# Kernel tuning notes

Hardware: AMD Instinct MI355X
Metric: run time of the kernel (lower is better)

The kernel has to match this reference:

```python
import jax, jax.numpy as jnp
import numpy as np

B, T, F, H, E, CTX = 64, 400, 80, 256, 256, 20


def setup_inputs() -> dict:
    ks = iter(jax.random.split(jax.random.key(0), 40))

    def p(shape):
        return jax.random.normal(next(ks), shape, jnp.float32) * 0.1

    inp = {"x": p((B, T, F))}
    inp["emb_W"], inp["emb_b"] = p((E, F)), p((E,))
    for name, din, dh in [("e1", F, H), ("e2", H, H), ("e3", H, H),
                          ("d1", 2 * E, H), ("d2", H, H), ("d3", H, F)]:
        inp[name + "_Wih"] = p((4 * dh, din))
        inp[name + "_Whh"] = p((4 * dh, dh))
        inp[name + "_b"] = p((4 * dh,))  # fused b_ih + b_hh
    inp["key_W"], inp["key_b"] = p((E, H)), p((E,))
    inp["val_W"], inp["val_b"] = p((E, H)), p((E,))
    inp["epoch"] = 5  # unused when isTrain=False (no teacher forcing)
    return inp


def _lstm(xin, hc, Wih, Whh, b):
    h, c = hc
    g = xin @ Wih.T + h @ Whh.T + b
    i, f, gg, o = jnp.split(g, 4, axis=-1)  # torch gate order i,f,g,o
    c = jax.nn.sigmoid(f) * c + jax.nn.sigmoid(i) * jnp.tanh(gg)
    h = jax.nn.sigmoid(o) * jnp.tanh(c)
    return (h, c)


def _forward(x, emb_W, emb_b, e1_Wih, e1_Whh, e1_b, e2_Wih, e2_Whh, e2_b,
             e3_Wih, e3_Whh, e3_b, d1_Wih, d1_Whh, d1_b, d2_Wih, d2_Whh, d2_b,
             d3_Wih, d3_Whh, d3_b, key_W, key_b, val_W, val_b):
    Bb = x.shape[0]
    z = lambda d: (jnp.zeros((Bb, d), x.dtype), jnp.zeros((Bb, d), x.dtype))

    def encoder(enc, xin):
        e1, e2, e3 = enc
        e1 = _lstm(xin, e1, e1_Wih, e1_Whh, e1_b)
        e2 = _lstm(e1[0], e2, e2_Wih, e2_Whh, e2_b)
        e3 = _lstm(e2[0], e3, e3_Wih, e3_Whh, e3_b)
        k = e3[0] @ key_W.T + key_b
        v = e3[0] @ val_W.T + val_b
        return (e1, e2, e3), k, v

    def decoder(dec, emb, ctx):
        d1, d2, d3 = dec
        din = jnp.concatenate([emb, ctx], axis=-1)  # [B, 2E]
        d1 = _lstm(din, d1, d1_Wih, d1_Whh, d1_b)
        d2 = _lstm(d1[0], d2, d2_Wih, d2_Whh, d2_b)
        d3 = _lstm(d2[0], d3, d3_Wih, d3_Whh, d3_b)
        return (d1, d2, d3)

    # phase 1: encoder warmup over steps 0..CTX-1
    def p1(enc, xt):
        enc, k, v = encoder(enc, xt)
        return enc, (k, v)

    enc, (ks_, vs_) = jax.lax.scan(p1, (z(H), z(H), z(H)),
                                   jnp.swapaxes(x[:, :CTX], 0, 1))
    kbuf = jnp.swapaxes(ks_, 0, 1)  # [B, CTX, E]: keys for steps 0..CTX-1
    vbuf = jnp.swapaxes(vs_, 0, 1)

    # step i == CTX: first decoder step; context = current value (values[-1])
    enc, k20, v20 = encoder(enc, x[:, CTX])
    kbuf = jnp.concatenate([kbuf[:, 1:], k20[:, None]], axis=1)
    vbuf = jnp.concatenate([vbuf[:, 1:], v20[:, None]], axis=1)
    emb = x[:, CTX - 1] @ emb_W.T + emb_b
    dec = decoder((z(H), z(H), z(F)), emb, v20)
    out20 = dec[2][0]  # [B, F]

    def p2(carry, _):
        enc, dec, kbuf, vbuf, last = carry
        enc, k, v = encoder(enc, last)           # encoder_input = prev decoder out
        emb = last @ emb_W.T + emb_b             # embedding of prev decoder out
        q = dec[1][0]                            # decoder2 hidden from prev step
        attn = jax.nn.softmax(jnp.einsum('bke,be->bk', kbuf, q), axis=-1)
        ctx = jnp.einsum('bk,bke->be', attn, vbuf)
        dec = decoder(dec, emb, ctx)
        kbuf = jnp.concatenate([kbuf[:, 1:], k[:, None]], axis=1)
        vbuf = jnp.concatenate([vbuf[:, 1:], v[:, None]], axis=1)
        out = dec[2][0]
        return (enc, dec, kbuf, vbuf, out), out

    _, outs = jax.lax.scan(p2, (enc, dec, kbuf, vbuf, out20), None,
                           length=T - CTX - 1)
    # [B, T-CTX, F] = [B, 380, 80]
    return jnp.concatenate([out20[:, None], jnp.swapaxes(outs, 0, 1)], axis=1)


def reference(x, emb_W, emb_b, e1_Wih, e1_Whh, e1_b, e2_Wih, e2_Whh, e2_b,
              e3_Wih, e3_Whh, e3_b, d1_Wih, d1_Whh, d1_b, d2_Wih, d2_Whh, d2_b,
              d3_Wih, d3_Whh, d3_b, key_W, key_b, val_W, val_b, epoch):
    return _forward(x, emb_W, emb_b, e1_Wih, e1_Whh, e1_b, e2_Wih, e2_Whh, e2_b,
                    e3_Wih, e3_Whh, e3_b, d1_Wih, d1_Whh, d1_b, d2_Wih, d2_Whh,
                    d2_b, d3_Wih, d3_Whh, d3_b, key_W, key_b, val_W, val_b)
```

## Files before the change

### kernel.cpp

```cpp
#include <hip/hip_runtime.h>

typedef short bf16x8 __attribute__((ext_vector_type(8)));
typedef float f32x4 __attribute__((ext_vector_type(4)));

#define DEV static __device__ __forceinline__
#define SCOPE_AGENT __HIP_MEMORY_SCOPE_AGENT

DEV unsigned short f2bf(float f) {
  unsigned u = __float_as_uint(f);
  unsigned r = u + 0x7fffu + ((u >> 16) & 1u);
  return (unsigned short)(r >> 16);
}
DEV float bf2f(unsigned short h) { return __uint_as_float(((unsigned)h) << 16); }
DEV void f2hilo(float f, unsigned short& hi, unsigned short& lo) {
  hi = f2bf(f);
  lo = f2bf(f - bf2f(hi));
}
DEV float sigm(float x) { return 1.f / (1.f + __expf(-x)); }
DEV float tanh_(float x) {
  x = fminf(15.f, fmaxf(-15.f, x));
  float e = __expf(2.f * x);
  return (e - 1.f) / (e + 1.f);
}

DEV void st_sc_u16(unsigned short* p, unsigned short v) {
  __hip_atomic_store(p, v, __ATOMIC_RELAXED, SCOPE_AGENT);
}
DEV void st_sc_f32(float* p, float v) {
  __hip_atomic_store(p, v, __ATOMIC_RELAXED, SCOPE_AGENT);
}
DEV void st_sc_u64(unsigned long long* p, unsigned long long v) {
  __hip_atomic_store(p, v, __ATOMIC_RELAXED, SCOPE_AGENT);
}
DEV unsigned long long ld_sc_u64(const unsigned long long* p) {
  return __hip_atomic_load((unsigned long long*)p, __ATOMIC_RELAXED, SCOPE_AGENT);
}
DEV unsigned ld_sc_u32(const unsigned* p) {
  return __hip_atomic_load((unsigned*)p, __ATOMIC_RELAXED, SCOPE_AGENT);
}
DEV void vm_drain() { asm volatile("s_waitcnt vmcnt(0)" ::: "memory"); }

constexpr size_t WE1 = 1024 * 352, WE2 = 1024 * 512, WE3 = 1024 * 512,
                 WD1 = 1024 * 768, WD2 = 1024 * 512, WD3 = 320 * 352,
                 WKEY = 256 * 256, WVAL = 256 * 256, WEMB = 256 * 96;
constexpr size_t E1HI = 0, E1LO = E1HI + WE1, E2HI = E1LO + WE1, E2LO = E2HI + WE2,
                 E3HI = E2LO + WE2, E3LO = E3HI + WE3, D1HI = E3LO + WE3, D1LO = D1HI + WD1,
                 D2HI = D1LO + WD1, D2LO = D2HI + WD2, D3HI = D2LO + WD2, D3LO = D3HI + WD3,
                 KHI = D3LO + WD3, KLO = KHI + WKEY, VHI = KLO + WKEY, VLO = VHI + WVAL,
                 EMHI = VLO + WVAL, EMLO = EMHI + WEMB, WTOT = EMLO + WEMB;

constexpr size_t XPAD_ELEMS = (size_t)400 * 64 * 96;
constexpr size_t XPAD_HI_B = WTOT * 2;
constexpr size_t XPAD_LO_B = XPAD_HI_B + XPAD_ELEMS * 2;
constexpr size_t STATE_B = XPAD_LO_B + XPAD_ELEMS * 2;

constexpr size_t H256_SZB = (size_t)2 * 2 * 64 * 256 * 2;
constexpr size_t HE1 = 0, HE2 = H256_SZB, HE3 = 2 * H256_SZB, HD1 = 3 * H256_SZB,
                 HD2 = 4 * H256_SZB;
constexpr size_t HLAST = 5 * H256_SZB;
constexpr size_t HLAST_SZB = (size_t)2 * 2 * 64 * 96 * 2;
constexpr size_t BARO = HLAST + HLAST_SZB;
constexpr size_t STATE_BYTES = BARO + 9 * 400 * 4 + 64;

constexpr size_t RINGK_B = STATE_B + STATE_BYTES;
constexpr size_t RING_SZ = (size_t)22 * 64 * 256 * 4;
constexpr size_t RINGV_B = RINGK_B + RING_SZ;
constexpr size_t CTXH_B = RINGV_B + RING_SZ;
constexpr size_t CTXL_B = CTXH_B + (size_t)64 * 256 * 2;
constexpr size_t D1BP_B = CTXL_B + (size_t)64 * 256 * 2;
constexpr size_t WS_NEED = D1BP_B + 4096;

#define LE1 0
#define LE2 1
#define LE3 2
#define LKV 3
#define LAT 5
#define LD1 6
#define LD2 7
#define LD3 8

constexpr int NWG = 67;
constexpr int WGS = 256;

__global__ void prep_w(const float* __restrict__ wih, int din, const float* __restrict__ whh,
                       int dh, int rows, int dinp, int kp, unsigned short* __restrict__ whi,
                       unsigned short* __restrict__ wlo) {
  size_t idx = (size_t)blockIdx.x * 256 + threadIdx.x;
  size_t tot = (size_t)rows * kp;
  if (idx >= tot) return;
  int j = (int)(idx / kp), k = (int)(idx % kp);
  float v = 0.f;
  if (k < dinp) {
    if (k < din) v = wih[(size_t)j * din + k];
  } else {
    int k2 = k - dinp;
    if (k2 < dh) v = whh[(size_t)j * dh + k2];
  }
  unsigned short hi, lo;
  f2hilo(v, hi, lo);
  whi[idx] = hi;
  wlo[idx] = lo;
}

__global__ void prep_d1_w(const float* __restrict__ wih, const float* __restrict__ whh,
                          const float* __restrict__ embW, unsigned short* __restrict__ whi,
                          unsigned short* __restrict__ wlo) {
  size_t idx = (size_t)blockIdx.x * 256 + threadIdx.x;
  constexpr size_t tot = (size_t)1024 * 608;
  if (idx >= tot) return;
  int j = (int)(idx / 608), f = (int)(idx % 608);
  float v = 0.f;
  if (f < 96) {
    if (f < 80) {
      const float* wr = wih + (size_t)j * 512;
#pragma unroll 4
      for (int m = 0; m < 256; m++) v += wr[m] * embW[(size_t)m * 80 + f];
    }
  } else if (f < 352) {
    v = wih[(size_t)j * 512 + 256 + (f - 96)];
  } else {
    v = whh[(size_t)j * 256 + (f - 352)];
  }
  unsigned short hi, lo;
  f2hilo(v, hi, lo);
  whi[idx] = hi;
  wlo[idx] = lo;
}

__global__ void prep_d1_bias(const float* __restrict__ wih, const float* __restrict__ embb,
                             const float* __restrict__ d1b, float* __restrict__ out) {
  int j = blockIdx.x * 256 + threadIdx.x;
  if (j >= 1024) return;
  float v = d1b[j];
  const float* wr = wih + (size_t)j * 512;
#pragma unroll 4
  for (int m = 0; m < 256; m++) v += wr[m] * embb[m];
  out[j] = v;
}

__global__ void prep_x(const float* __restrict__ x, unsigned short* __restrict__ xh,
                       unsigned short* __restrict__ xl) {
  size_t idx = (size_t)blockIdx.x * 256 + threadIdx.x;
  if (idx >= XPAD_ELEMS) return;
  int t = (int)(idx / 6144), rbf = (int)(idx % 6144), b = rbf / 96, f = rbf % 96;
  float v = (f < 80) ? x[(size_t)b * 32000 + (size_t)t * 80 + f] : 0.f;
  unsigned short hi, lo;
  f2hilo(v, hi, lo);
  xh[idx] = hi;
  xl[idx] = lo;
}


template <int COLS, int STRIDE>
DEV void copy_hl(unsigned short* lds, const unsigned short* hi, const unsigned short* lo,
                 int tid) {
  constexpr int CU64 = COLS / 4;
  constexpr int PER = 64 * CU64;
  constexpr int TOT = PER * 2;
  constexpr int loOff = 64 * STRIDE;
  for (int base = 0; base < TOT; base += WGS * 16) {
    unsigned long long v[16];
    int dst[16];
#pragma unroll
    for (int u = 0; u < 16; u++) {
      int i = base + u * WGS + tid;
      dst[u] = -1;
      if (i < TOT) {
        int pl = (i >= PER) ? 1 : 0;
        int j = pl ? (i - PER) : i;
        int row = j / CU64, cc = j - row * CU64;
        const unsigned long long* s = (const unsigned long long*)(pl ? lo : hi);
        v[u] = ld_sc_u64(s + j);
        dst[u] = (pl ? loOff : 0) + row * STRIDE + ((cc * 4) ^ ((row & 7) << 3));
      }
    }
#pragma unroll
    for (int u = 0; u < 16; u++)
      if (dst[u] >= 0) *(unsigned long long*)(lds + dst[u]) = v[u];
  }
}

DEV void mfma3(f32x4& acc, bf16x8 ah, bf16x8 al, bf16x8 bh, bf16x8 bl) {
  acc = __builtin_amdgcn_mfma_f32_16x16x32_bf16(ah, bh, acc, 0, 0, 0);
  acc = __builtin_amdgcn_mfma_f32_16x16x32_bf16(al, bh, acc, 0, 0, 0);
  acc = __builtin_amdgcn_mfma_f32_16x16x32_bf16(ah, bl, acc, 0, 0, 0);
}

DEV void zacc44(f32x4 (&a)[4][4]) {
#pragma unroll
  for (int g = 0; g < 4; g++)
#pragma unroll
    for (int m = 0; m < 4; m++) a[g][m] = f32x4{0.f, 0.f, 0.f, 0.f};
}

template <int STRIDE>
DEV void mfma_range(const unsigned short* lds, int lane, int ut, int H,
                    const unsigned short* __restrict__ Whi,
                    const unsigned short* __restrict__ Wlo, int Kp, int kwOff, int kbLo,
                    int kbHi, f32x4 (&acc)[4][4]) {
  const int col = lane & 15, kg = lane >> 4;
  constexpr int loOff = 64 * STRIDE;
  for (int kb = kbLo; kb < kbHi; kb++) {
    const int ka = kb * 32 + kg * 8;
    bf16x8 ah[4], al[4];
#pragma unroll
    for (int m = 0; m < 4; m++) {
      int row = m * 16 + col;
      int off = row * STRIDE + (ka ^ ((row & 7) << 3));
      ah[m] = *(const bf16x8*)(lds + off);
      al[m] = *(const bf16x8*)(lds + loOff + off);
    }
#pragma unroll
    for (int g = 0; g < 4; g++) {
      size_t wr = (size_t)(g * H + ut * 16 + col) * Kp + kwOff + ka;
      bf16x8 bh = *(const bf16x8*)(Whi + wr);
      bf16x8 bl = *(const bf16x8*)(Wlo + wr);
#pragma unroll
      for (int m = 0; m < 4; m++) mfma3(acc[g][m], ah[m], al[m], bh, bl);
    }
  }
}

template <int COLS, int STRIDE>
DEV void chunk_pass(unsigned short* lds, const unsigned short* hi, const unsigned short* lo,
                    int tid, int lane, int ut, int utActive, int H,
                    const unsigned short* __restrict__ Whi,
                    const unsigned short* __restrict__ Wlo, int Kp, int kwOff, int half,
                    f32x4 (&acc)[4][4]) {
  __syncthreads();
  copy_hl<COLS, STRIDE>(lds, hi, lo, tid);
  __syncthreads();
  constexpr int NKB = COLS / 32;
  const int lo_kb = half ? (NKB + 1) / 2 : 0;
  const int hi_kb = half ? NKB : (NKB + 1) / 2;
  if (utActive) mfma_range<STRIDE>(lds, lane, ut, H, Whi, Wlo, Kp, kwOff, lo_kb, hi_kb, acc);
}

DEV void reduce_pair(unsigned short* lds, int lane, int pair, int half, f32x4 (&acc)[4][4]) {
  float* red = (float*)lds;
  const int base = (pair * 64 + lane) * 68;
  __syncthreads();
  if (half) {
#pragma unroll
    for (int g = 0; g < 4; g++)
#pragma unroll
      for (int m = 0; m < 4; m++)
#pragma unroll
        for (int r = 0; r < 4; r++) red[base + (g * 4 + m) * 4 + r] = acc[g][m][r];
  }
  __syncthreads();
  if (!half) {
#pragma unroll
    for (int g = 0; g < 4; g++)
#pragma unroll
      for (int m = 0; m < 4; m++)
#pragma unroll
        for (int r = 0; r < 4; r++) acc[g][m][r] += red[base + (g * 4 + m) * 4 + r];
  }
}

DEV void cell_update(int lane, int ut, int H, int Hpad, const float* __restrict__ bias,
                     f32x4 (&acc)[4][4], float (&c)[4][4], unsigned short* hwhi,
                     unsigned short* hwlo, float* outp) {
  const int col = lane & 15, kg = lane >> 4;
  const int u = ut * 16 + col;
  const float bi = bias[u], bff = bias[H + u], bg = bias[2 * H + u], bo = bias[3 * H + u];
#pragma unroll
  for (int m = 0; m < 4; m++)
#pragma unroll
    for (int r = 0; r < 4; r++) {
      int b = m * 16 + kg * 4 + r;
      float gi = acc[0][m][r] + bi, gf = acc[1][m][r] + bff;
      float gg = acc[2][m][r] + bg, go = acc[3][m][r] + bo;
      float cn = sigm(gf) * c[m][r] + sigm(gi) * tanh_(gg);
      float hh = sigm(go) * tanh_(cn);
      c[m][r] = cn;
      unsigned short hi, lo;
      f2hilo(hh, hi, lo);
      st_sc_u16(hwhi + b * Hpad + u, hi);
      st_sc_u16(hwlo + b * Hpad + u, lo);
      if (outp) outp[(size_t)b * 30400 + u] = hh;
    }
}

template <int K, int STRIDE>
DEV void mfma_lin(const unsigned short* lds, int lane, int jt,
                  const unsigned short* __restrict__ Whi,
                  const unsigned short* __restrict__ Wlo, int Kp, f32x4 (&acc)[4]) {
  const int col = lane & 15, kg = lane >> 4;
  constexpr int loOff = 64 * STRIDE;
#pragma unroll
  for (int kb = 0; kb < K; kb += 32) {
    const int ka = kb + kg * 8;
    size_t wr = (size_t)(jt * 16 + col) * Kp + ka;
    bf16x8 bh = *(const bf16x8*)(Whi + wr);
    bf16x8 bl = *(const bf16x8*)(Wlo + wr);
#pragma unroll
    for (int m = 0; m < 4; m++) {
      int row = m * 16 + col;
      int off = row * STRIDE + (ka ^ ((row & 7) << 3));
      bf16x8 ah = *(const bf16x8*)(lds + off);
      bf16x8 al = *(const bf16x8*)(lds + loOff + off);
      mfma3(acc[m], ah, al, bh, bl);
    }
  }
}

DEV void spin3(const unsigned* p0, unsigned t0, const unsigned* p1, unsigned t1,
               const unsigned* p2, unsigned t2) {
  for (;;) {
    unsigned a = p0 ? ld_sc_u32(p0) : 0xFFFFFFFFu;
    unsigned b = p1 ? ld_sc_u32(p1) : 0xFFFFFFFFu;
    unsigned c = p2 ? ld_sc_u32(p2) : 0xFFFFFFFFu;
    if (a >= t0 && b >= t1 && c >= t2) return;
    __builtin_amdgcn_s_sleep(1);
  }
}

__global__ void __launch_bounds__(WGS, 1)
seq_main(const float* e1b, const float* e2b, const float* e3b, const float* d2b,
         const float* d3b, const float* keyb, const float* valb, float* dout,
         unsigned char* ws) {
  __shared__ unsigned short lds_s[32768];
  unsigned short* lds = lds_s;

  const int wg = blockIdx.x, tid = threadIdx.x;
  const int wv = tid >> 6, lane = tid & 63;
  const int pair = wv >> 1, half = wv & 1;

  unsigned short* W = (unsigned short*)ws;
  const unsigned short* xh = (const unsigned short*)(ws + XPAD_HI_B);
  const unsigned short* xl = (const unsigned short*)(ws + XPAD_LO_B);
  unsigned char* st = ws + STATE_B;
  float* ringk = (float*)(ws + RINGK_B);
  float* ringv = (float*)(ws + RINGV_B);
  unsigned short* ctxh = (unsigned short*)(ws + CTXH_B);
  unsigned short* ctxl = (unsigned short*)(ws + CTXL_B);
  const float* d1bp = (const float*)(ws + D1BP_B);
  unsigned* C = (unsigned*)(st + BARO);
  auto CNT = [&](int l, int tt) { return C + l * 400 + tt; };

  auto hb = [&](size_t off, int par, int hl, int Hpad) {
    return (unsigned short*)(st + off) + (size_t)(par * 2 + hl) * 64 * Hpad;
  };
  auto bump = [&](int l, int tt) {
    if (tid == 0) __hip_atomic_fetch_add(CNT(l, tt), 1u, __ATOMIC_RELAXED, SCOPE_AGENT);
  };

  if (wg < 8) {
    const int ut = wg * 2 + pair;
    float c[4][4] = {{0.f}};
    for (int t = 0; t < 400; ++t) {
      const int p = t & 1, q = p ^ 1;
      f32x4 acc[4][4];
      zacc44(acc);
      if (tid == 0 && t >= 1) spin3(CNT(LE1, t - 1), 8, nullptr, 0, nullptr, 0);
      chunk_pass<256, 256>(lds, hb(HE1, q, 0, 256), hb(HE1, q, 1, 256), tid, lane, ut, 1, 256,
                           W + E1HI, W + E1LO, 352, 96, half, acc);
      if (tid == 0)
        spin3(t >= 21 ? CNT(LD3, t - 1) : nullptr, 3, t >= 2 ? CNT(LE2, t - 2) : nullptr, 8,
              nullptr, 0);
      if (t <= 20)
        chunk_pass<96, 128>(lds, xh + (size_t)t * 6144, xl + (size_t)t * 6144, tid, lane, ut, 1,
                            256, W + E1HI, W + E1LO, 352, 0, half, acc);
      else
        chunk_pass<96, 128>(lds, hb(HLAST, q, 0, 96), hb(HLAST, q, 1, 96), tid, lane, ut, 1,
                            256, W + E1HI, W + E1LO, 352, 0, half, acc);
      reduce_pair(lds, lane, pair, half, acc);
      if (!half)
        cell_update(lane, ut, 256, 256, e1b, acc, c, hb(HE1, p, 0, 256), hb(HE1, p, 1, 256),
                    nullptr);
      vm_drain();
      __syncthreads();
      bump(LE1, t);
    }
  } else if (wg < 16) {
    const int ut = (wg - 8) * 2 + pair;
    float c[4][4] = {{0.f}};
    for (int t = 0; t < 400; ++t) {
      const int p = t & 1, q = p ^ 1;
      f32x4 acc[4][4];
      zacc44(acc);
      if (tid == 0 && t >= 1) spin3(CNT(LE2, t - 1), 8, nullptr, 0, nullptr, 0);
      chunk_pass<256, 256>(lds, hb(HE2, q, 0, 256), hb(HE2, q, 1, 256), tid, lane, ut, 1, 256,
                           W + E2HI, W + E2LO, 512, 256, half, acc);
      if (tid == 0)
        spin3(CNT(LE1, t), 8, t >= 2 ? CNT(LE3, t - 2) : nullptr, 8, nullptr, 0);
      chunk_pass<256, 256>(lds, hb(HE1, p, 0, 256), hb(HE1, p, 1, 256), tid, lane, ut, 1, 256,
                           W + E2HI, W + E2LO, 512, 0, half, acc);
      reduce_pair(lds, lane, pair, half, acc);
      if (!half)
        cell_update(lane, ut, 256, 256, e2b, acc, c, hb(HE2, p, 0, 256), hb(HE2, p, 1, 256),
                    nullptr);
      vm_drain();
      __syncthreads();
      bump(LE2, t);
    }
  } else if (wg < 24) {
    const int ut = (wg - 16) * 2 + pair;
    float c[4][4] = {{0.f}};
    for (int t = 0; t < 400; ++t) {
      const int p = t & 1, q = p ^ 1;
      f32x4 acc[4][4];
      zacc44(acc);
      if (tid == 0 && t >= 1) spin3(CNT(LE3, t - 1), 8, nullptr, 0, nullptr, 0);
      chunk_pass<256, 256>(lds, hb(HE3, q, 0, 256), hb(HE3, q, 1, 256), tid, lane, ut, 1, 256,
                           W + E3HI, W + E3LO, 512, 256, half, acc);
      if (tid == 0)
        spin3(CNT(LE2, t), 8, t >= 2 ? CNT(LKV, t - 2) : nullptr, 8, nullptr, 0);
      chunk_pass<256, 256>(lds, hb(HE2, p, 0, 256), hb(HE2, p, 1, 256), tid, lane, ut, 1, 256,
                           W + E3HI, W + E3LO, 512, 0, half, acc);
      reduce_pair(lds, lane, pair, half, acc);
      if (!half)
        cell_update(lane, ut, 256, 256, e3b, acc, c, hb(HE3, p, 0, 256), hb(HE3, p, 1, 256),
                    nullptr);
      vm_drain();
      __syncthreads();
      bump(LE3, t);
    }
  } else if (wg < 32) {
    const bool isKey = wg < 28;
    const unsigned short* Whi = W + (isKey ? KHI : VHI);
    const unsigned short* Wlo = W + (isKey ? KLO : VLO);
    const float* bias = isKey ? keyb : valb;
    float* ring = isKey ? ringk : ringv;
    const int jt = (wg - (isKey ? 24 : 28)) * 4 + wv;
    const int col = lane & 15, kg = lane >> 4;
    for (int t = 0; t < 400; ++t) {
      const int p = t & 1;
      const int slot = t % 22;
      if (tid == 0)
        spin3(CNT(LE3, t), 8, t >= 22 ? CNT(LAT, t - 2) : nullptr, 16, nullptr, 0);
      __syncthreads();
      copy_hl<256, 256>(lds, hb(HE3, p, 0, 256), hb(HE3, p, 1, 256), tid);
      __syncthreads();
      float* outp = ring + (size_t)slot * 64 * 256;
      f32x4 acc[4];
#pragma unroll
      for (int m = 0; m < 4; m++) acc[m] = f32x4{0.f, 0.f, 0.f, 0.f};
      mfma_lin<256, 256>(lds, lane, jt, Whi, Wlo, 256, acc);
      int j = jt * 16 + col;
      float bj = bias[j];
#pragma unroll
      for (int m = 0; m < 4; m++)
#pragma unroll
        for (int r = 0; r < 4; r++) {
          int b = m * 16 + kg * 4 + r;
          st_sc_f32(outp + (size_t)b * 256 + j, acc[m][r] + bj);
        }
      vm_drain();
      __syncthreads();
      bump(LKV, t);
    }
  } else if (wg < 48) {
    const int b = (wg - 32) * 4 + wv;
    for (int t = 20; t < 400; ++t) {
      const int q = (t & 1) ^ 1;
      if (t == 20) {
        if (tid == 0) spin3(CNT(LKV, 20), 8, nullptr, 0, nullptr, 0);
        __syncthreads();
        const unsigned long long* vp =
            (const unsigned long long*)(ringv + ((size_t)20 * 64 + b) * 256 + lane * 4);
        unsigned long long v0 = ld_sc_u64(vp), v1 = ld_sc_u64(vp + 1);
        float f[4] = {__uint_as_float((unsigned)v0), __uint_as_float((unsigned)(v0 >> 32)),
                      __uint_as_float((unsigned)v1), __uint_as_float((unsigned)(v1 >> 32))};
        unsigned short hi[4], lo[4];
#pragma unroll
        for (int j = 0; j < 4; j++) f2hilo(f[j], hi[j], lo[j]);
        unsigned long long ph = (unsigned long long)hi[0] | ((unsigned long long)hi[1] << 16) |
                                ((unsigned long long)hi[2] << 32) |
                                ((unsigned long long)hi[3] << 48);
        unsigned long long pl = (unsigned long long)lo[0] | ((unsigned long long)lo[1] << 16) |
                                ((unsigned long long)lo[2] << 32) |
                                ((unsigned long long)lo[3] << 48);
        st_sc_u64((unsigned long long*)(ctxh + b * 256 + lane * 4), ph);
        st_sc_u64((unsigned long long*)(ctxl + b * 256 + lane * 4), pl);
      } else {
        if (tid == 0)
          spin3(CNT(LKV, t - 1), 8, CNT(LD2, t - 1), 8, CNT(LD1, t - 1), 8);
        __syncthreads();
        const unsigned short* qh = hb(HD2, q, 0, 256);
        const unsigned short* ql = hb(HD2, q, 1, 256);
        unsigned long long hq = ld_sc_u64((const unsigned long long*)(qh + b * 256 + lane * 4));
        unsigned long long lq = ld_sc_u64((const unsigned long long*)(ql + b * 256 + lane * 4));
        float qv[4];
#pragma unroll
        for (int j = 0; j < 4; j++)
          qv[j] = bf2f((unsigned short)(hq >> (16 * j))) + bf2f((unsigned short)(lq >> (16 * j)));
        float s[20];
#pragma unroll
        for (int i = 0; i < 20; i++) {
          int slot = (t - 20 + i) % 22;
          const unsigned long long* kp =
              (const unsigned long long*)(ringk + ((size_t)slot * 64 + b) * 256 + lane * 4);
          unsigned long long k0 = ld_sc_u64(kp), k1 = ld_sc_u64(kp + 1);
          s[i] = __uint_as_float((unsigned)k0) * qv[0] +
                 __uint_as_float((unsigned)(k0 >> 32)) * qv[1] +
                 __uint_as_float((unsigned)k1) * qv[2] +
                 __uint_as_float((unsigned)(k1 >> 32)) * qv[3];
        }
#pragma unroll
        for (int off = 32; off >= 1; off >>= 1)
#pragma unroll
          for (int i = 0; i < 20; i++) s[i] += __shfl_xor(s[i], off, 64);
        float mx = s[0];
#pragma unroll
        for (int i = 1; i < 20; i++) mx = fmaxf(mx, s[i]);
        float den = 0.f;
#pragma unroll
        for (int i = 0; i < 20; i++) {
          s[i] = __expf(s[i] - mx);
          den += s[i];
        }
        float inv = 1.f / den;
        float a0 = 0.f, a1 = 0.f, a2 = 0.f, a3 = 0.f;
#pragma unroll
        for (int i = 0; i < 20; i++) {
          int slot = (t - 20 + i) % 22;
          const unsigned long long* vp =
              (const unsigned long long*)(ringv + ((size_t)slot * 64 + b) * 256 + lane * 4);
          unsigned long long v0 = ld_sc_u64(vp), v1 = ld_sc_u64(vp + 1);
          a0 += s[i] * __uint_as_float((unsigned)v0);
          a1 += s[i] * __uint_as_float((unsigned)(v0 >> 32));
          a2 += s[i] * __uint_as_float((unsigned)v1);
          a3 += s[i] * __uint_as_float((unsigned)(v1 >> 32));
        }
        float f[4] = {a0 * inv, a1 * inv, a2 * inv, a3 * inv};
        unsigned short hi[4], lo[4];
#pragma unroll
        for (int j = 0; j < 4; j++) f2hilo(f[j], hi[j], lo[j]);
        unsigned long long ph = (unsigned long long)hi[0] | ((unsigned long long)hi[1] << 16) |
                                ((unsigned long long)hi[2] << 32) |
                                ((unsigned long long)hi[3] << 48);
        unsigned long long pl = (unsigned long long)lo[0] | ((unsigned long long)lo[1] << 16) |
                                ((unsigned long long)lo[2] << 32) |
                                ((unsigned long long)lo[3] << 48);
        st_sc_u64((unsigned long long*)(ctxh + b * 256 + lane * 4), ph);
        st_sc_u64((unsigned long long*)(ctxl + b * 256 + lane * 4), pl);
      }
      vm_drain();
      __syncthreads();
      bump(LAT, t);
    }
  } else if (wg < 56) {
    const int ut = (wg - 48) * 2 + pair;
    float c[4][4] = {{0.f}};
    for (int t = 20; t < 400; ++t) {
      const int p = t & 1, q = p ^ 1;
      f32x4 acc[4][4];
      zacc44(acc);
      if (tid == 0 && t >= 21) spin3(CNT(LD1, t - 1), 8, nullptr, 0, nullptr, 0);
      chunk_pass<256, 256>(lds, hb(HD1, q, 0, 256), hb(HD1, q, 1, 256), tid, lane, ut, 1, 256,
                           W + D1HI, W + D1LO, 608, 352, half, acc);
      if (tid == 0 && t >= 21) spin3(CNT(LD3, t - 1), 3, nullptr, 0, nullptr, 0);
      if (t == 20)
        chunk_pass<96, 128>(lds, xh + (size_t)19 * 6144, xl + (size_t)19 * 6144, tid, lane, ut,
                            1, 256, W + D1HI, W + D1LO, 608, 0, half, acc);
      else
        chunk_pass<96, 128>(lds, hb(HLAST, q, 0, 96), hb(HLAST, q, 1, 96), tid, lane, ut, 1,
                            256, W + D1HI, W + D1LO, 608, 0, half, acc);
      if (tid == 0) spin3(CNT(LAT, t), 16, nullptr, 0, nullptr, 0);
      chunk_pass<256, 256>(lds, ctxh, ctxl, tid, lane, ut, 1, 256, W + D1HI, W + D1LO, 608, 96,
                           half, acc);
      reduce_pair(lds, lane, pair, half, acc);
      if (!half)
        cell_update(lane, ut, 256, 256, d1bp, acc, c, hb(HD1, p, 0, 256), hb(HD1, p, 1, 256),
                    nullptr);
      vm_drain();
      __syncthreads();
      bump(LD1, t);
    }
  } else if (wg < 64) {
    const int ut = (wg - 56) * 2 + pair;
    float c[4][4] = {{0.f}};
    for (int t = 20; t < 400; ++t) {
      const int p = t & 1, q = p ^ 1;
      f32x4 acc[4][4];
      zacc44(acc);
      if (tid == 0 && t >= 21) spin3(CNT(LD2, t - 1), 8, nullptr, 0, nullptr, 0);
      chunk_pass<256, 256>(lds, hb(HD2, q, 0, 256), hb(HD2, q, 1, 256), tid, lane, ut, 1, 256,
                           W + D2HI, W + D2LO, 512, 256, half, acc);
      if (tid == 0) spin3(CNT(LD1, t), 8, nullptr, 0, nullptr, 0);
      chunk_pass<256, 256>(lds, hb(HD1, p, 0, 256), hb(HD1, p, 1, 256), tid, lane, ut, 1, 256,
                           W + D2HI, W + D2LO, 512, 0, half, acc);
      reduce_pair(lds, lane, pair, half, acc);
      if (!half)
        cell_update(lane, ut, 256, 256, d2b, acc, c, hb(HD2, p, 0, 256), hb(HD2, p, 1, 256),
                    nullptr);
      vm_drain();
      __syncthreads();
      bump(LD2, t);
    }
  } else {
    const int ut = (wg - 64) * 2 + pair;
    const int utActive = (ut < 5) ? 1 : 0;
    float c[4][4] = {{0.f}};
    for (int t = 20; t < 400; ++t) {
      const int p = t & 1, q = p ^ 1;
      f32x4 acc[4][4];
      zacc44(acc);
      if (tid == 0 && t >= 21) spin3(CNT(LD3, t - 1), 3, nullptr, 0, nullptr, 0);
      chunk_pass<96, 128>(lds, hb(HLAST, q, 0, 96), hb(HLAST, q, 1, 96), tid, lane, ut, utActive,
                          80, W + D3HI, W + D3LO, 352, 256, half, acc);
      if (tid == 0) spin3(CNT(LD2, t), 8, nullptr, 0, nullptr, 0);
      chunk_pass<256, 256>(lds, hb(HD2, p, 0, 256), hb(HD2, p, 1, 256), tid, lane, ut, utActive,
                           80, W + D3HI, W + D3LO, 352, 0, half, acc);
      reduce_pair(lds, lane, pair, half, acc);
      if (!half && utActive)
        cell_update(lane, ut, 80, 96, d3b, acc, c, hb(HLAST, p, 0, 96), hb(HLAST, p, 1, 96),
                    dout + (size_t)(t - 20) * 80);
      vm_drain();
      __syncthreads();
      bump(LD3, t);
    }
  }
}

extern "C" void kernel_launch(void* const* d_in, const int* in_sizes, int n_in, void* d_out,
                              int out_size, void* d_ws, size_t ws_size, hipStream_t stream) {
  if (ws_size < WS_NEED) return;

  const float* x = (const float*)d_in[0];
  const float* embW = (const float*)d_in[1];
  const float* embB = (const float*)d_in[2];
  const float* e1Wih = (const float*)d_in[3];
  const float* e1Whh = (const float*)d_in[4];
  const float* e1B = (const float*)d_in[5];
  const float* e2Wih = (const float*)d_in[6];
  const float* e2Whh = (const float*)d_in[7];
  const float* e2B = (const float*)d_in[8];
  const float* e3Wih = (const float*)d_in[9];
  const float* e3Whh = (const float*)d_in[10];
  const float* e3B = (const float*)d_in[11];
  const float* d1Wih = (const float*)d_in[12];
  const float* d1Whh = (const float*)d_in[13];
  const float* d1B = (const float*)d_in[14];
  const float* d2Wih = (const float*)d_in[15];
  const float* d2Whh = (const float*)d_in[16];
  const float* d2B = (const float*)d_in[17];
  const float* d3Wih = (const float*)d_in[18];
  const float* d3Whh = (const float*)d_in[19];
  const float* d3B = (const float*)d_in[20];
  const float* keyW = (const float*)d_in[21];
  const float* keyB = (const float*)d_in[22];
  const float* valW = (const float*)d_in[23];
  const float* valB = (const float*)d_in[24];

  unsigned char* ws = (unsigned char*)d_ws;
  unsigned short* W = (unsigned short*)ws;
  float* doutf = (float*)d_out;

  auto launch_w = [&](const float* wih, int din, const float* whh, int dh, int rows, int dinp,
                      int kp, size_t offhi, size_t offlo) {
    size_t tot = (size_t)rows * kp;
    int blocks = (int)((tot + 255) / 256);
    prep_w<<<blocks, 256, 0, stream>>>(wih, din, whh, dh, rows, dinp, kp, W + offhi, W + offlo);
  };
  launch_w(e1Wih, 80, e1Whh, 256, 1024, 96, 352, E1HI, E1LO);
  launch_w(e2Wih, 256, e2Whh, 256, 1024, 256, 512, E2HI, E2LO);
  launch_w(e3Wih, 256, e3Whh, 256, 1024, 256, 512, E3HI, E3LO);
  launch_w(d2Wih, 256, d2Whh, 256, 1024, 256, 512, D2HI, D2LO);
  launch_w(d3Wih, 256, d3Whh, 80, 320, 256, 352, D3HI, D3LO);
  launch_w(keyW, 256, nullptr, 0, 256, 256, 256, KHI, KLO);
// ... 14 lines not shown
```

Before: 14.99 ms.

## Fuse key/value projection into attention workgroups, partitioned by batch

Replaces the separate key/value projection stage (8 workgroups) with projection work done inside the 16 attention workgroups, each handling 4 batch rows. Each attention workgroup computes K/V for its own batch rows, keeps the newest step's K/V in LDS, and uses that LDS copy for the latest attention slot. This removes a cross-workgroup barrier hop and ring round-trip on the critical path. The trade-off is that the projection now runs serially inside the attention step, and encoder3 gains a wait on attention progress. The copy_hl unroll is also doubled.

```diff
diff --git a/kernel.cpp b/kernel.cpp
--- a/kernel.cpp
+++ b/kernel.cpp
@@ -73,13 +73,12 @@
 #define LE1 0
 #define LE2 1
 #define LE3 2
-#define LKV 3
 #define LAT 5
 #define LD1 6
 #define LD2 7
 #define LD3 8
 
-constexpr int NWG = 67;
+constexpr int NWG = 59;
 constexpr int WGS = 256;
 
 __global__ void prep_w(const float* __restrict__ wih, int din, const float* __restrict__ whh,
@@ -158,11 +157,11 @@
   constexpr int PER = 64 * CU64;
   constexpr int TOT = PER * 2;
   constexpr int loOff = 64 * STRIDE;
-  for (int base = 0; base < TOT; base += WGS * 16) {
-    unsigned long long v[16];
-    int dst[16];
-#pragma unroll
-    for (int u = 0; u < 16; u++) {
+  for (int base = 0; base < TOT; base += WGS * 32) {
+    unsigned long long v[32];
+    int dst[32];
+#pragma unroll
+    for (int u = 0; u < 32; u++) {
       int i = base + u * WGS + tid;
       dst[u] = -1;
       if (i < TOT) {
@@ -175,7 +174,7 @@
       }
     }
 #pragma unroll
-    for (int u = 0; u < 16; u++)
+    for (int u = 0; u < 32; u++)
       if (dst[u] >= 0) *(unsigned long long*)(lds + dst[u]) = v[u];
   }
 }
@@ -281,29 +280,6 @@
       st_sc_u16(hwlo + b * Hpad + u, lo);
       if (outp) outp[(size_t)b * 30400 + u] = hh;
     }
-}
-
-template <int K, int STRIDE>
-DEV void mfma_lin(const unsigned short* lds, int lane, int jt,
-                  const unsigned short* __restrict__ Whi,
-                  const unsigned short* __restrict__ Wlo, int Kp, f32x4 (&acc)[4]) {
-  const int col = lane & 15, kg = lane >> 4;
-  constexpr int loOff = 64 * STRIDE;
-#pragma unroll
-  for (int kb = 0; kb < K; kb += 32) {
-    const int ka = kb + kg * 8;
-    size_t wr = (size_t)(jt * 16 + col) * Kp + ka;
-    bf16x8 bh = *(const bf16x8*)(Whi + wr);
-    bf16x8 bl = *(const bf16x8*)(Wlo + wr);
-#pragma unroll
-    for (int m = 0; m < 4; m++) {
-      int row = m * 16 + col;
-      int off = row * STRIDE + (ka ^ ((row & 7) << 3));
-      bf16x8 ah = *(const bf16x8*)(lds + off);
-      bf16x8 al = *(const bf16x8*)(lds + loOff + off);
-      mfma3(acc[m], ah, al, bh, bl);
-    }
-  }
 }
 
 DEV void spin3(const unsigned* p0, unsigned t0, const unsigned* p1, unsigned t1,
@@ -406,11 +382,12 @@
       if (tid == 0 && t >= 1) spin3(CNT(LE3, t - 1), 8, nullptr, 0, nullptr, 0);
       chunk_pass<256, 256>(lds, hb(HE3, q, 0, 256), hb(HE3, q, 1, 256), tid, lane, ut, 1, 256,
                            W + E3HI, W + E3LO, 512, 256, half, acc);
-      if (tid == 0)
-        spin3(CNT(LE2, t), 8, t >= 2 ? CNT(LKV, t - 2) : nullptr, 8, nullptr, 0);
+      if (tid == 0) spin3(CNT(LE2, t), 8, nullptr, 0, nullptr, 0);
       chunk_pass<256, 256>(lds, hb(HE2, p, 0, 256), hb(HE2, p, 1, 256), tid, lane, ut, 1, 256,
                            W + E3HI, W + E3LO, 512, 0, half, acc);
       reduce_pair(lds, lane, pair, half, acc);
+      if (tid == 0 && t >= 1) spin3(CNT(LAT, t - 1), 16, nullptr, 0, nullptr, 0);
+      __syncthreads();
       if (!half)
         cell_update(lane, ut, 256, 256, e3b, acc, c, hb(HE3, p, 0, 256), hb(HE3, p, 1, 256),
                     nullptr);
@@ -418,52 +395,66 @@
       __syncthreads();
       bump(LE3, t);
     }
-  } else if (wg < 32) {
-    const bool isKey = wg < 28;
-    const unsigned short* Whi = W + (isKey ? KHI : VHI);
-    const unsigned short* Wlo = W + (isKey ? KLO : VLO);
-    const float* bias = isKey ? keyb : valb;
-    float* ring = isKey ? ringk : ringv;
-    const int jt = (wg - (isKey ? 24 : 28)) * 4 + wv;
-    const int col = lane & 15, kg = lane >> 4;
+  } else if (wg < 40) {
+    const int b0 = (wg - 24) * 4;
+    float* kvx = (float*)(lds + 8192);
     for (int t = 0; t < 400; ++t) {
-      const int p = t & 1;
-      const int slot = t % 22;
-      if (tid == 0)
-        spin3(CNT(LE3, t), 8, t >= 22 ? CNT(LAT, t - 2) : nullptr, 16, nullptr, 0);
-      __syncthreads();
-      copy_hl<256, 256>(lds, hb(HE3, p, 0, 256), hb(HE3, p, 1, 256), tid);
-      __syncthreads();
-      float* outp = ring + (size_t)slot * 64 * 256;
-      f32x4 acc[4];
-#pragma unroll
-      for (int m = 0; m < 4; m++) acc[m] = f32x4{0.f, 0.f, 0.f, 0.f};
-      mfma_lin<256, 256>(lds, lane, jt, Whi, Wlo, 256, acc);
-      int j = jt * 16 + col;
-      float bj = bias[j];
-#pragma unroll
-      for (int m = 0; m < 4; m++)
-#pragma unroll
-        for (int r = 0; r < 4; r++) {
-          int b = m * 16 + kg * 4 + r;
-          st_sc_f32(outp + (size_t)b * 256 + j, acc[m][r] + bj);
+      const int s = (t <= 20) ? t : t - 1;
+      const int ps = s & 1;
+      const bool doKV = (t != 21);
+      if (tid == 0) {
+        if (t <= 20)
+          spin3(CNT(LE3, t), 8, nullptr, 0, nullptr, 0);
+        else
+          spin3(CNT(LE3, t - 1), 8, CNT(LD2, t - 1), 8, CNT(LD1, t - 1), 8);
+      }
+      __syncthreads();
+      if (doKV) {
+        for (int i = tid; i < 512; i += WGS) {
+          int pl = i >> 8, j = i & 255, row = j >> 6, cc = j & 63;
+          const unsigned long long* srcp =
+              (const unsigned long long*)hb(HE3, ps, pl, 256) + (size_t)(b0 + row) * 64 + cc;
+          unsigned long long v = ld_sc_u64(srcp);
+          *(unsigned long long*)(lds + pl * 4096 + row * 256 +
+                                 ((cc * 4) ^ ((row & 7) << 3))) = v;
         }
-      vm_drain();
-      __syncthreads();
-      bump(LKV, t);
-    }
-  } else if (wg < 48) {
-    const int b = (wg - 32) * 4 + wv;
-    for (int t = 20; t < 400; ++t) {
-      const int q = (t & 1) ^ 1;
+        __syncthreads();
+        const int slot = s % 22;
+        const int col = lane & 15, kg = lane >> 4;
+        for (int jj = 0; jj < 8; ++jj) {
+          int jt = wv * 8 + jj;
+          bool isK = jt < 16;
+          int j = (isK ? jt : jt - 16) * 16 + col;
+          const unsigned short* Whi = W + (isK ? KHI : VHI);
+          const unsigned short* Wlo = W + (isK ? KLO : VLO);
+          f32x4 acc = f32x4{0.f, 0.f, 0.f, 0.f};
+          for (int kb = 0; kb < 8; kb++) {
+            int ka = kb * 32 + kg * 8;
+            int offA = col * 256 + (ka ^ ((col & 7) << 3));
+            bf16x8 ah = *(const bf16x8*)(lds + offA);
+            bf16x8 al = *(const bf16x8*)(lds + 4096 + offA);
+            size_t wr = (size_t)j * 256 + ka;
+            bf16x8 bh = *(const bf16x8*)(Whi + wr);
+            bf16x8 bl = *(const bf16x8*)(Wlo + wr);
+            mfma3(acc, ah, al, bh, bl);
+          }
+          if (kg == 0) {
+            float bj = (isK ? keyb : valb)[j];
+            float* ringp = (isK ? ringk : ringv) + (size_t)slot * 64 * 256;
+#pragma unroll
+            for (int r = 0; r < 4; r++) {
+              float v = acc[r] + bj;
+              st_sc_f32(ringp + (size_t)(b0 + r) * 256 + j, v);
+              kvx[r * 512 + (isK ? j : 256 + j)] = v;
+            }
+          }
+        }
+        __syncthreads();
+      }
       if (t == 20) {
-        if (tid == 0) spin3(CNT(LKV, 20), 8, nullptr, 0, nullptr, 0);
-        __syncthreads();
-        const unsigned long long* vp =
-            (const unsigned long long*)(ringv + ((size_t)20 * 64 + b) * 256 + lane * 4);
-        unsigned long long v0 = ld_sc_u64(vp), v1 = ld_sc_u64(vp + 1);
-        float f[4] = {__uint_as_float((unsigned)v0), __uint_as_float((unsigned)(v0 >> 32)),
-                      __uint_as_float((unsigned)v1), __uint_as_float((unsigned)(v1 >> 32))};
+        float f[4];
+#pragma unroll
+        for (int j = 0; j < 4; j++) f[j] = kvx[wv * 512 + 256 + lane * 4 + j];
         unsigned short hi[4], lo[4];
 #pragma unroll
         for (int j = 0; j < 4; j++) f2hilo(f[j], hi[j], lo[j]);
@@ -473,58 +464,67 @@
         unsigned long long pl = (unsigned long long)lo[0] | ((unsigned long long)lo[1] << 16) |
                                 ((unsigned long long)lo[2] << 32) |
                                 ((unsigned long long)lo[3] << 48);
-        st_sc_u64((unsigned long long*)(ctxh + b * 256 + lane * 4), ph);
-        st_sc_u64((unsigned long long*)(ctxl + b * 256 + lane * 4), pl);
-      } else {
-        if (tid == 0)
-          spin3(CNT(LKV, t - 1), 8, CNT(LD2, t - 1), 8, CNT(LD1, t - 1), 8);
-        __syncthreads();
-        const unsigned short* qh = hb(HD2, q, 0, 256);
-        const unsigned short* ql = hb(HD2, q, 1, 256);
+        st_sc_u64((unsigned long long*)(ctxh + (b0 + wv) * 256 + lane * 4), ph);
+        st_sc_u64((unsigned long long*)(ctxl + (b0 + wv) * 256 + lane * 4), pl);
+      } else if (t >= 21) {
+        const int b = b0 + wv;
+        const int qp = (t & 1) ^ 1;
+        const unsigned short* qh = hb(HD2, qp, 0, 256);
+        const unsigned short* ql = hb(HD2, qp, 1, 256);
         unsigned long long hq = ld_sc_u64((const unsigned long long*)(qh + b * 256 + lane * 4));
         unsigned long long lq = ld_sc_u64((const unsigned long long*)(ql + b * 256 + lane * 4));
         float qv[4];
 #pragma unroll
         for (int j = 0; j < 4; j++)
           qv[j] = bf2f((unsigned short)(hq >> (16 * j))) + bf2f((unsigned short)(lq >> (16 * j)));
-        float s[20];
-#pragma unroll
-        for (int i = 0; i < 20; i++) {
+        float sArr[20];
+#pragma unroll
+        for (int i = 0; i < 19; i++) {
           int slot = (t - 20 + i) % 22;
           const unsigned long long* kp =
               (const unsigned long long*)(ringk + ((size_t)slot * 64 + b) * 256 + lane * 4);
           unsigned long long k0 = ld_sc_u64(kp), k1 = ld_sc_u64(kp + 1);
-          s[i] = __uint_as_float((unsigned)k0) * qv[0] +
-                 __uint_as_float((unsigned)(k0 >> 32)) * qv[1] +
-                 __uint_as_float((unsigned)k1) * qv[2] +
-                 __uint_as_float((unsigned)(k1 >> 32)) * qv[3];
+          sArr[i] = __uint_as_float((unsigned)k0) * qv[0] +
+                    __uint_as_float((unsigned)(k0 >> 32)) * qv[1] +
+                    __uint_as_float((unsigned)k1) * qv[2] +
+                    __uint_as_float((unsigned)(k1 >> 32)) * qv[3];
         }
+        {
+          float acc19 = 0.f;
+#pragma unroll
+          for (int j = 0; j < 4; j++) acc19 += kvx[wv * 512 + lane * 4 + j] * qv[j];
+          sArr[19] = acc19;
+        }
 #pragma unroll
         for (int off = 32; off >= 1; off >>= 1)
 #pragma unroll
-          for (int i = 0; i < 20; i++) s[i] += __shfl_xor(s[i], off, 64);
-        float mx = s[0];
-#pragma unroll
-        for (int i = 1; i < 20; i++) mx = fmaxf(mx, s[i]);
+          for (int i = 0; i < 20; i++) sArr[i] += __shfl_xor(sArr[i], off, 64);
+        float mx = sArr[0];
+#pragma unroll
+        for (int i = 1; i < 20; i++) mx = fmaxf(mx, sArr[i]);
         float den = 0.f;
 #pragma unroll
         for (int i = 0; i < 20; i++) {
-          s[i] = __expf(s[i] - mx);
-          den += s[i];
+          sArr[i] = __expf(sArr[i] - mx);
+          den += sArr[i];
         }
         float inv = 1.f / den;
         float a0 = 0.f, a1 = 0.f, a2 = 0.f, a3 = 0.f;
 #pragma unroll
-        for (int i = 0; i < 20; i++) {
+        for (int i = 0; i < 19; i++) {
           int slot = (t - 20 + i) % 22;
           const unsigned long long* vp =
               (const unsigned long long*)(ringv + ((size_t)slot * 64 + b) * 256 + lane * 4);
           unsigned long long v0 = ld_sc_u64(vp), v1 = ld_sc_u64(vp + 1);
-          a0 += s[i] * __uint_as_float((unsigned)v0);
-          a1 += s[i] * __uint_as_float((unsigned)(v0 >> 32));
-          a2 += s[i] * __uint_as_float((unsigned)v1);
-          a3 += s[i] * __uint_as_float((unsigned)(v1 >> 32));
+          a0 += sArr[i] * __uint_as_float((unsigned)v0);
+          a1 += sArr[i] * __uint_as_float((unsigned)(v0 >> 32));
+          a2 += sArr[i] * __uint_as_float((unsigned)v1);
+          a3 += sArr[i] * __uint_as_float((unsigned)(v1 >> 32));
         }
+        a0 += sArr[19] * kvx[wv * 512 + 256 + lane * 4 + 0];
+        a1 += sArr[19] * kvx[wv * 512 + 256 + lane * 4 + 1];
+        a2 += sArr[19] * kvx[wv * 512 + 256 + lane * 4 + 2];
+        a3 += sArr[19] * kvx[wv * 512 + 256 + lane * 4 + 3];
         float f[4] = {a0 * inv, a1 * inv, a2 * inv, a3 * inv};
         unsigned short hi[4], lo[4];
 #pragma unroll
@@ -542,8 +542,8 @@
       __syncthreads();
       bump(LAT, t);
     }
-  } else if (wg < 56) {
-    const int ut = (wg - 48) * 2 + pair;
+  } else if (wg < 48) {
+    const int ut = (wg - 40) * 2 + pair;
     float c[4][4] = {{0.f}};
     for (int t = 20; t < 400; ++t) {
       const int p = t & 1, q = p ^ 1;
@@ -570,8 +570,8 @@
       __syncthreads();
       bump(LD1, t);
     }
-  } else if (wg < 64) {
-    const int ut = (wg - 56) * 2 + pair;
+  } else if (wg < 56) {
+    const int ut = (wg - 48) * 2 + pair;
     float c[4][4] = {{0.f}};
     for (int t = 20; t < 400; ++t) {
       const int p = t & 1, q = p ^ 1;
@@ -592,7 +592,7 @@
       bump(LD2, t);
     }
   } else {
-    const int ut = (wg - 64) * 2 + pair;
+    const int ut = (wg - 56) * 2 + pair;
     const int utActive = (ut < 5) ? 1 : 0;
     float c[4][4] = {{0.f}};
     for (int t = 20; t < 400; ++t) {
```

New measurement: 18.30 ms. +22.1%, slower.

## Stage LSTM hidden outputs in LDS, double-buffer context, and relax attention dependency

Applied to the files above, without the earlier changes.

Hidden-state outputs from the LSTM cell update are first written to an LDS staging area and then stored to global memory as coalesced 64-bit writes, replacing scattered 16-bit stores. The attention context buffer is double-buffered by timestep parity, so the attention workgroups no longer wait for decoder layer 1 of the previous step before overwriting the context. The LDS copy loop is also unrolled to 32 loads per pass. These changes target global store efficiency and the serial dependency chain on the recurrent critical path, at the cost of an extra barrier per step and more registers in the copy loop.

```diff
diff --git a/kernel.cpp b/kernel.cpp
--- a/kernel.cpp
+++ b/kernel.cpp
@@ -66,8 +66,8 @@
 constexpr size_t RING_SZ = (size_t)22 * 64 * 256 * 4;
 constexpr size_t RINGV_B = RINGK_B + RING_SZ;
 constexpr size_t CTXH_B = RINGV_B + RING_SZ;
-constexpr size_t CTXL_B = CTXH_B + (size_t)64 * 256 * 2;
-constexpr size_t D1BP_B = CTXL_B + (size_t)64 * 256 * 2;
+constexpr size_t CTXL_B = CTXH_B + (size_t)2 * 64 * 256 * 2;
+constexpr size_t D1BP_B = CTXL_B + (size_t)2 * 64 * 256 * 2;
 constexpr size_t WS_NEED = D1BP_B + 4096;
 
 #define LE1 0
@@ -81,6 +81,7 @@
 
 constexpr int NWG = 67;
 constexpr int WGS = 256;
+constexpr int HSTG = 20480;
 
 __global__ void prep_w(const float* __restrict__ wih, int din, const float* __restrict__ whh,
                        int dh, int rows, int dinp, int kp, unsigned short* __restrict__ whi,
@@ -158,11 +159,11 @@
   constexpr int PER = 64 * CU64;
   constexpr int TOT = PER * 2;
   constexpr int loOff = 64 * STRIDE;
-  for (int base = 0; base < TOT; base += WGS * 16) {
-    unsigned long long v[16];
-    int dst[16];
-#pragma unroll
-    for (int u = 0; u < 16; u++) {
+  for (int base = 0; base < TOT; base += WGS * 32) {
+    unsigned long long v[32];
+    int dst[32];
+#pragma unroll
+    for (int u = 0; u < 32; u++) {
       int i = base + u * WGS + tid;
       dst[u] = -1;
       if (i < TOT) {
@@ -175,7 +176,7 @@
       }
     }
 #pragma unroll
-    for (int u = 0; u < 16; u++)
+    for (int u = 0; u < 32; u++)
       if (dst[u] >= 0) *(unsigned long long*)(lds + dst[u]) = v[u];
   }
 }
@@ -259,11 +260,12 @@
   }
 }
 
-DEV void cell_update(int lane, int ut, int H, int Hpad, const float* __restrict__ bias,
-                     f32x4 (&acc)[4][4], float (&c)[4][4], unsigned short* hwhi,
-                     unsigned short* hwlo, float* outp) {
+DEV void cell_update_lds(unsigned short* hstage, int lane, int pairIdx, int ut, int H,
+                         const float* __restrict__ bias, f32x4 (&acc)[4][4], float (&c)[4][4],
+                         float* outp) {
   const int col = lane & 15, kg = lane >> 4;
   const int u = ut * 16 + col;
+  const int uloc = pairIdx * 16 + col;
   const float bi = bias[u], bff = bias[H + u], bg = bias[2 * H + u], bo = bias[3 * H + u];
 #pragma unroll
   for (int m = 0; m < 4; m++)
@@ -277,10 +279,23 @@
       c[m][r] = cn;
       unsigned short hi, lo;
       f2hilo(hh, hi, lo);
-      st_sc_u16(hwhi + b * Hpad + u, hi);
-      st_sc_u16(hwlo + b * Hpad + u, lo);
+      hstage[b * 32 + uloc] = hi;
+      hstage[2048 + b * 32 + uloc] = lo;
       if (outp) outp[(size_t)b * 30400 + u] = hh;
     }
+}
+
+DEV void store_h(const unsigned short* hstage, int tid, unsigned short* hwhi,
+                 unsigned short* hwlo, int u0, int Hpad, int ncols) {
+  const int rowu64 = ncols >> 2;
+  const int per = 64 * rowu64;
+  for (int i = tid; i < per * 2; i += WGS) {
+    int pl = (i >= per) ? 1 : 0;
+    int j = pl ? i - per : i;
+    int b = j / rowu64, cc = j - b * rowu64;
+    unsigned long long v = *(const unsigned long long*)(hstage + pl * 2048 + b * 32 + cc * 4);
+    st_sc_u64((unsigned long long*)((pl ? hwlo : hwhi) + (size_t)b * Hpad + u0) + cc, v);
+  }
 }
 
 template <int K, int STRIDE>
@@ -349,6 +364,7 @@
 
   if (wg < 8) {
     const int ut = wg * 2 + pair;
+    const int u0 = wg * 32;
     float c[4][4] = {{0.f}};
     for (int t = 0; t < 400; ++t) {
       const int p = t & 1, q = p ^ 1;
@@ -367,15 +383,16 @@
         chunk_pass<96, 128>(lds, hb(HLAST, q, 0, 96), hb(HLAST, q, 1, 96), tid, lane, ut, 1,
                             256, W + E1HI, W + E1LO, 352, 0, half, acc);
       reduce_pair(lds, lane, pair, half, acc);
-      if (!half)
-        cell_update(lane, ut, 256, 256, e1b, acc, c, hb(HE1, p, 0, 256), hb(HE1, p, 1, 256),
-                    nullptr);
+      if (!half) cell_update_lds(lds + HSTG, lane, pair, ut, 256, e1b, acc, c, nullptr);
+      __syncthreads();
+      store_h(lds + HSTG, tid, hb(HE1, p, 0, 256), hb(HE1, p, 1, 256), u0, 256, 32);
       vm_drain();
       __syncthreads();
       bump(LE1, t);
     }
   } else if (wg < 16) {
     const int ut = (wg - 8) * 2 + pair;
+    const int u0 = (wg - 8) * 32;
     float c[4][4] = {{0.f}};
     for (int t = 0; t < 400; ++t) {
       const int p = t & 1, q = p ^ 1;
@@ -389,15 +406,16 @@
       chunk_pass<256, 256>(lds, hb(HE1, p, 0, 256), hb(HE1, p, 1, 256), tid, lane, ut, 1, 256,
                            W + E2HI, W + E2LO, 512, 0, half, acc);
       reduce_pair(lds, lane, pair, half, acc);
-      if (!half)
-        cell_update(lane, ut, 256, 256, e2b, acc, c, hb(HE2, p, 0, 256), hb(HE2, p, 1, 256),
-                    nullptr);
+      if (!half) cell_update_lds(lds + HSTG, lane, pair, ut, 256, e2b, acc, c, nullptr);
+      __syncthreads();
+      store_h(lds + HSTG, tid, hb(HE2, p, 0, 256), hb(HE2, p, 1, 256), u0, 256, 32);
       vm_drain();
       __syncthreads();
       bump(LE2, t);
     }
   } else if (wg < 24) {
     const int ut = (wg - 16) * 2 + pair;
+    const int u0 = (wg - 16) * 32;
     float c[4][4] = {{0.f}};
     for (int t = 0; t < 400; ++t) {
       const int p = t & 1, q = p ^ 1;
@@ -411,9 +429,9 @@
       chunk_pass<256, 256>(lds, hb(HE2, p, 0, 256), hb(HE2, p, 1, 256), tid, lane, ut, 1, 256,
                            W + E3HI, W + E3LO, 512, 0, half, acc);
       reduce_pair(lds, lane, pair, half, acc);
-      if (!half)
-        cell_update(lane, ut, 256, 256, e3b, acc, c, hb(HE3, p, 0, 256), hb(HE3, p, 1, 256),
-                    nullptr);
+      if (!half) cell_update_lds(lds + HSTG, lane, pair, ut, 256, e3b, acc, c, nullptr);
+      __syncthreads();
+      store_h(lds + HSTG, tid, hb(HE3, p, 0, 256), hb(HE3, p, 1, 256), u0, 256, 32);
       vm_drain();
       __syncthreads();
       bump(LE3, t);
@@ -455,7 +473,8 @@
   } else if (wg < 48) {
     const int b = (wg - 32) * 4 + wv;
     for (int t = 20; t < 400; ++t) {
-      const int q = (t & 1) ^ 1;
+      unsigned short* ch = ctxh + (size_t)(t & 1) * 64 * 256;
+      unsigned short* cl = ctxl + (size_t)(t & 1) * 64 * 256;
       if (t == 20) {
         if (tid == 0) spin3(CNT(LKV, 20), 8, nullptr, 0, nullptr, 0);
         __syncthreads();
@@ -473,44 +492,44 @@
         unsigned long long pl = (unsigned long long)lo[0] | ((unsigned long long)lo[1] << 16) |
                                 ((unsigned long long)lo[2] << 32) |
                                 ((unsigned long long)lo[3] << 48);
-        st_sc_u64((unsigned long long*)(ctxh + b * 256 + lane * 4), ph);
-        st_sc_u64((unsigned long long*)(ctxl + b * 256 + lane * 4), pl);
+        st_sc_u64((unsigned long long*)(ch + b * 256 + lane * 4), ph);
+        st_sc_u64((unsigned long long*)(cl + b * 256 + lane * 4), pl);
       } else {
-        if (tid == 0)
-          spin3(CNT(LKV, t - 1), 8, CNT(LD2, t - 1), 8, CNT(LD1, t - 1), 8);
+        if (tid == 0) spin3(CNT(LKV, t - 1), 8, CNT(LD2, t - 1), 8, nullptr, 0);
         __syncthreads();
-        const unsigned short* qh = hb(HD2, q, 0, 256);
-        const unsigned short* ql = hb(HD2, q, 1, 256);
+        const int qp = (t & 1) ^ 1;
+        const unsigned short* qh = hb(HD2, qp, 0, 256);
+        const unsigned short* ql = hb(HD2, qp, 1, 256);
         unsigned long long hq = ld_sc_u64((const unsigned long long*)(qh + b * 256 + lane * 4));
         unsigned long long lq = ld_sc_u64((const unsigned long long*)(ql + b * 256 + lane * 4));
         float qv[4];
 #pragma unroll
         for (int j = 0; j < 4; j++)
           qv[j] = bf2f((unsigned short)(hq >> (16 * j))) + bf2f((unsigned short)(lq >> (16 * j)));
-        float s[20];
+        float sArr[20];
 #pragma unroll
         for (int i = 0; i < 20; i++) {
           int slot = (t - 20 + i) % 22;
           const unsigned long long* kp =
               (const unsigned long long*)(ringk + ((size_t)slot * 64 + b) * 256 + lane * 4);
           unsigned long long k0 = ld_sc_u64(kp), k1 = ld_sc_u64(kp + 1);
-          s[i] = __uint_as_float((unsigned)k0) * qv[0] +
-                 __uint_as_float((unsigned)(k0 >> 32)) * qv[1] +
-                 __uint_as_float((unsigned)k1) * qv[2] +
-                 __uint_as_float((unsigned)(k1 >> 32)) * qv[3];
+          sArr[i] = __uint_as_float((unsigned)k0) * qv[0] +
+                    __uint_as_float((unsigned)(k0 >> 32)) * qv[1] +
+                    __uint_as_float((unsigned)k1) * qv[2] +
+                    __uint_as_float((unsigned)(k1 >> 32)) * qv[3];
         }
 #pragma unroll
         for (int off = 32; off >= 1; off >>= 1)
 #pragma unroll
-          for (int i = 0; i < 20; i++) s[i] += __shfl_xor(s[i], off, 64);
-        float mx = s[0];
-#pragma unroll
-        for (int i = 1; i < 20; i++) mx = fmaxf(mx, s[i]);
+          for (int i = 0; i < 20; i++) sArr[i] += __shfl_xor(sArr[i], off, 64);
+        float mx = sArr[0];
+#pragma unroll
+        for (int i = 1; i < 20; i++) mx = fmaxf(mx, sArr[i]);
         float den = 0.f;
 #pragma unroll
         for (int i = 0; i < 20; i++) {
-          s[i] = __expf(s[i] - mx);
-          den += s[i];
+          sArr[i] = __expf(sArr[i] - mx);
+          den += sArr[i];
         }
         float inv = 1.f / den;
         float a0 = 0.f, a1 = 0.f, a2 = 0.f, a3 = 0.f;
@@ -520,10 +539,10 @@
           const unsigned long long* vp =
               (const unsigned long long*)(ringv + ((size_t)slot * 64 + b) * 256 + lane * 4);
           unsigned long long v0 = ld_sc_u64(vp), v1 = ld_sc_u64(vp + 1);
-          a0 += s[i] * __uint_as_float((unsigned)v0);
-          a1 += s[i] * __uint_as_float((unsigned)(v0 >> 32));
-          a2 += s[i] * __uint_as_float((unsigned)v1);
-          a3 += s[i] * __uint_as_float((unsigned)(v1 >> 32));
+          a0 += sArr[i] * __uint_as_float((unsigned)v0);
+          a1 += sArr[i] * __uint_as_float((unsigned)(v0 >> 32));
+          a2 += sArr[i] * __uint_as_float((unsigned)v1);
+          a3 += sArr[i] * __uint_as_float((unsigned)(v1 >> 32));
         }
         float f[4] = {a0 * inv, a1 * inv, a2 * inv, a3 * inv};
         unsigned short hi[4], lo[4];
@@ -535,8 +554,8 @@
         unsigned long long pl = (unsigned long long)lo[0] | ((unsigned long long)lo[1] << 16) |
                                 ((unsigned long long)lo[2] << 32) |
                                 ((unsigned long long)lo[3] << 48);
-        st_sc_u64((unsigned long long*)(ctxh + b * 256 + lane * 4), ph);
-        st_sc_u64((unsigned long long*)(ctxl + b * 256 + lane * 4), pl);
+        st_sc_u64((unsigned long long*)(ch + b * 256 + lane * 4), ph);
+        st_sc_u64((unsigned long long*)(cl + b * 256 + lane * 4), pl);
       }
       vm_drain();
       __syncthreads();
@@ -544,6 +563,7 @@
     }
   } else if (wg < 56) {
     const int ut = (wg - 48) * 2 + pair;
+    const int u0 = (wg - 48) * 32;
     float c[4][4] = {{0.f}};
     for (int t = 20; t < 400; ++t) {
       const int p = t & 1, q = p ^ 1;
@@ -560,18 +580,19 @@
         chunk_pass<96, 128>(lds, hb(HLAST, q, 0, 96), hb(HLAST, q, 1, 96), tid, lane, ut, 1,
                             256, W + D1HI, W + D1LO, 608, 0, half, acc);
       if (tid == 0) spin3(CNT(LAT, t), 16, nullptr, 0, nullptr, 0);
-      chunk_pass<256, 256>(lds, ctxh, ctxl, tid, lane, ut, 1, 256, W + D1HI, W + D1LO, 608, 96,
-                           half, acc);
+      chunk_pass<256, 256>(lds, ctxh + (size_t)p * 64 * 256, ctxl + (size_t)p * 64 * 256, tid,
+                           lane, ut, 1, 256, W + D1HI, W + D1LO, 608, 96, half, acc);
       reduce_pair(lds, lane, pair, half, acc);
-      if (!half)
-        cell_update(lane, ut, 256, 256, d1bp, acc, c, hb(HD1, p, 0, 256), hb(HD1, p, 1, 256),
-                    nullptr);
+      if (!half) cell_update_lds(lds + HSTG, lane, pair, ut, 256, d1bp, acc, c, nullptr);
+      __syncthreads();
+      store_h(lds + HSTG, tid, hb(HD1, p, 0, 256), hb(HD1, p, 1, 256), u0, 256, 32);
       vm_drain();
       __syncthreads();
       bump(LD1, t);
     }
   } else if (wg < 64) {
     const int ut = (wg - 56) * 2 + pair;
+    const int u0 = (wg - 56) * 32;
     float c[4][4] = {{0.f}};
     for (int t = 20; t < 400; ++t) {
       const int p = t & 1, q = p ^ 1;
@@ -584,9 +605,9 @@
       chunk_pass<256, 256>(lds, hb(HD1, p, 0, 256), hb(HD1, p, 1, 256), tid, lane, ut, 1, 256,
                            W + D2HI, W + D2LO, 512, 0, half, acc);
       reduce_pair(lds, lane, pair, half, acc);
-      if (!half)
-        cell_update(lane, ut, 256, 256, d2b, acc, c, hb(HD2, p, 0, 256), hb(HD2, p, 1, 256),
-                    nullptr);
+      if (!half) cell_update_lds(lds + HSTG, lane, pair, ut, 256, d2b, acc, c, nullptr);
+      __syncthreads();
+      store_h(lds + HSTG, tid, hb(HD2, p, 0, 256), hb(HD2, p, 1, 256), u0, 256, 32);
       vm_drain();
       __syncthreads();
       bump(LD2, t);
@@ -594,6 +615,8 @@
   } else {
     const int ut = (wg - 64) * 2 + pair;
     const int utActive = (ut < 5) ? 1 : 0;
+    const int u0 = (wg - 64) * 32;
+    const int ncols = (wg == 66) ? 16 : 32;
     float c[4][4] = {{0.f}};
     for (int t = 20; t < 400; ++t) {
       const int p = t & 1, q = p ^ 1;
@@ -607,8 +630,10 @@
                            80, W + D3HI, W + D3LO, 352, 0, half, acc);
       reduce_pair(lds, lane, pair, half, acc);
       if (!half && utActive)
-        cell_update(lane, ut, 80, 96, d3b, acc, c, hb(HLAST, p, 0, 96), hb(HLAST, p, 1, 96),
-                    dout + (size_t)(t - 20) * 80);
+        cell_update_lds(lds + HSTG, lane, pair, ut, 80, d3b, acc, c,
+                        dout + (size_t)(t - 20) * 80);
+      __syncthreads();
+      store_h(lds + HSTG, tid, hb(HLAST, p, 0, 96), hb(HLAST, p, 1, 96), u0, 96, ncols);
       vm_drain();
       __syncthreads();
       bump(LD3, t);
```

New measurement: 15.63 ms. 4.3% more time.
